# Kernel tuning notes

Hardware: AMD Instinct MI355X
Metric: run time of the kernel (lower is better)

The kernel has to match this reference:

```python
import jax, jax.numpy as jnp
import numpy as np

E = 500000          # num edges
V_IN = 128          # node feature dim
E_IN = 64           # edge feature dim
U_IN = 64           # global feature dim
HID = 256           # hidden_dim
NG = 512            # num graphs
CAT = 2 * V_IN + E_IN + U_IN  # 448


def setup_inputs() -> dict:
    key = jax.random.key(0)
    ks = jax.random.split(key, 8)
    return {
        "src": jax.random.normal(ks[0], (E, V_IN), dtype=jnp.float32),
        "dest": jax.random.normal(ks[1], (E, V_IN), dtype=jnp.float32),
        "edge_attr": jax.random.normal(ks[2], (E, E_IN), dtype=jnp.float32),
        "u": jax.random.normal(ks[3], (NG, U_IN), dtype=jnp.float32),
        "batch": jax.random.randint(ks[4], (E,), 0, NG, dtype=jnp.int64),
        "W1": jax.random.normal(ks[5], (CAT, HID), dtype=jnp.float32) * (1.0 / np.sqrt(CAT)),
        "b1": jnp.zeros((HID,), dtype=jnp.float32),
        "W2": jax.random.normal(ks[6], (HID, HID), dtype=jnp.float32) * (1.0 / np.sqrt(HID)),
        "b2": jnp.zeros((HID,), dtype=jnp.float32),
    }


def reference(src, dest, edge_attr, u, batch, W1, b1, W2, b2):
    # gather per-edge global features, concat, then 2-layer MLP with ReLU
    x = jnp.concatenate([src, dest, edge_attr, u[batch]], axis=1)  # [E, CAT]
    h = jax.nn.relu(x @ W1 + b1)                                   # [E, HID]
    return h @ W2 + b2                                             # [E, HID]
```

## Files before the change

kernel.cpp:

```cpp
#include <hip/hip_runtime.h>
#include <hip/hip_bf16.h>

#define E_EDGES 500000
#define V_IN 128
#define E_IN 64
#define U_IN 64
#define NG 512
#define HID 256
#define CAT 384
#define BM 64
#define BK 32
#define NCHUNK1 12
#define NCHUNK2 8
#define TILE 8192

typedef short short8 __attribute__((ext_vector_type(8)));
typedef float f32x4 __attribute__((ext_vector_type(4)));

static __device__ __forceinline__ short f2bf(float f) {
  unsigned u = __builtin_bit_cast(unsigned, f);
  u += 0x7fffu + ((u >> 16) & 1u);
  return (short)(u >> 16);
}

static __device__ __forceinline__ void gload_lds16(const void* g, void* l) {
  __builtin_amdgcn_global_load_lds(
      (const __attribute__((address_space(1))) unsigned int*)g,
      (unsigned int __attribute__((address_space(3)))*)l, 16, 0, 0);
}

static __device__ __forceinline__ void stage_w(const short* gsrc, short* lbase,
                                               int w, int l) {
#pragma unroll
  for (int i = 0; i < 4; ++i) {
    int off = (w * 4 + i) * 1024;
    gload_lds16((const char*)gsrc + off + l * 16, (char*)lbase + off);
  }
}

__global__ void prep_weights(const float* __restrict__ W1,
                             const float* __restrict__ W2,
                             short* __restrict__ w1t, short* __restrict__ w2t) {
  int idx = blockIdx.x * 256 + threadIdx.x;
  if (idx < CAT * HID) {
    int kc = idx >> 13;
    int rem = idx & (TILE - 1);
    int n = rem >> 5, kk = rem & 31;
    int swz = ((((kk >> 3) ^ (n & 3)) << 3) | (kk & 7));
    w1t[kc * TILE + n * 32 + swz] = f2bf(W1[(size_t)(kc * 32 + kk) * HID + n]);
  } else if (idx < CAT * HID + HID * HID) {
    int j = idx - CAT * HID;
    int kc = j >> 13;
    int rem = j & (TILE - 1);
    int n = rem >> 5, kk = rem & 31;
    int swz = ((((kk >> 3) ^ (n & 3)) << 3) | (kk & 7));
    w2t[kc * TILE + n * 32 + swz] = f2bf(W2[(size_t)(kc * 32 + kk) * HID + n]);
  }
}

__global__ __launch_bounds__(256, 2) void edge_mlp(
    const float* __restrict__ src, const float* __restrict__ dst,
    const float* __restrict__ edg, const float* __restrict__ u,
    const int* __restrict__ batch,
    const float* __restrict__ b1, const float* __restrict__ b2,
    const short* __restrict__ w1t, const short* __restrict__ w2t,
    float* __restrict__ out) {
  __shared__ short xs[BM][40];
  __shared__ short wsl[2][TILE];
  __shared__ short hs[BM][264];
  __shared__ float biasLds[2 * HID];

  const int t = threadIdx.x;
  const int l = t & 63;
  const int wc = t >> 6;
  const int l15 = l & 15, lg = l >> 4;
  const int r0 = blockIdx.x * BM;

  stage_w(w1t, wsl[0], wc, l);

  const int srow = t >> 2;
  const int cq = (t & 3) << 3;
  int gr = r0 + srow;
  if (gr >= E_EDGES) gr = E_EDGES - 1;
  int bi = batch[gr];
  bi = bi < 0 ? 0 : (bi >= NG ? NG - 1 : bi);
  const float* uptr = u + (size_t)bi * U_IN;
  const float* csrc[NCHUNK1] = {
      src + (size_t)gr * V_IN + cq,        src + (size_t)gr * V_IN + 32 + cq,
      src + (size_t)gr * V_IN + 64 + cq,   src + (size_t)gr * V_IN + 96 + cq,
      dst + (size_t)gr * V_IN + cq,        dst + (size_t)gr * V_IN + 32 + cq,
      dst + (size_t)gr * V_IN + 64 + cq,   dst + (size_t)gr * V_IN + 96 + cq,
      edg + (size_t)gr * E_IN + cq,        edg + (size_t)gr * E_IN + 32 + cq,
      uptr + cq,                           uptr + 32 + cq};

  f32x4 xv0, xv1;
  {
    const f32x4* p = (const f32x4*)csrc[0];
    xv0 = p[0]; xv1 = p[1];
  }

  biasLds[t] = b1[t];
  biasLds[t + HID] = b2[t];

  f32x4 acc[4][4];
#pragma unroll
  for (int m = 0; m < 4; ++m)
#pragma unroll
    for (int n = 0; n < 4; ++n)
#pragma unroll
      for (int j = 0; j < 4; ++j) acc[m][n][j] = 0.f;

#pragma unroll
  for (int kc = 0; kc < NCHUNK1; ++kc) {
    {
      short8 v;
      v[0] = f2bf(xv0[0]); v[1] = f2bf(xv0[1]); v[2] = f2bf(xv0[2]); v[3] = f2bf(xv0[3]);
      v[4] = f2bf(xv1[0]); v[5] = f2bf(xv1[1]); v[6] = f2bf(xv1[2]); v[7] = f2bf(xv1[3]);
      *(short8*)&xs[srow][cq] = v;
    }
    __syncthreads();

    f32x4 nx0, nx1;
    if (kc < NCHUNK1 - 1) {
      stage_w(w1t + (kc + 1) * TILE, wsl[(kc + 1) & 1], wc, l);
      const f32x4* p = (const f32x4*)csrc[kc + 1];
      nx0 = p[0]; nx1 = p[1];
    } else {
      stage_w(w2t, wsl[0], wc, l);
    }

    const short* wcur = wsl[kc & 1];
    short8 a[4], b[4];
#pragma unroll
    for (int m = 0; m < 4; ++m)
      a[m] = *(const short8*)&xs[m * 16 + l15][lg * 8];
#pragma unroll
    for (int n = 0; n < 4; ++n) {
      int nn = wc * 64 + n * 16 + l15;
      int blk = lg ^ (nn & 3);
      b[n] = *(const short8*)&wcur[nn * 32 + blk * 8];
    }
#pragma unroll
    for (int m = 0; m < 4; ++m)
#pragma unroll
      for (int n = 0; n < 4; ++n)
        acc[m][n] = __builtin_amdgcn_mfma_f32_16x16x32_bf16(a[m], b[n], acc[m][n], 0, 0, 0);

    __syncthreads();
    if (kc < NCHUNK1 - 1) { xv0 = nx0; xv1 = nx1; }
  }

#pragma unroll
  for (int n = 0; n < 4; ++n) {
    int col = wc * 64 + n * 16 + l15;
    float bv = biasLds[col];
#pragma unroll
    for (int m = 0; m < 4; ++m)
#pragma unroll
      for (int j = 0; j < 4; ++j) {
        int row = m * 16 + lg * 4 + j;
        float hv = acc[m][n][j] + bv;
        hs[row][col] = f2bf(fmaxf(hv, 0.f));
      }
  }

#pragma unroll
  for (int m = 0; m < 4; ++m)
#pragma unroll
    for (int n = 0; n < 4; ++n)
#pragma unroll
      for (int j = 0; j < 4; ++j) acc[m][n][j] = 0.f;

  __syncthreads();

#pragma unroll
  for (int kc = 0; kc < NCHUNK2; ++kc) {
    if (kc < NCHUNK2 - 1)
      stage_w(w2t + (kc + 1) * TILE, wsl[(kc + 1) & 1], wc, l);

    const short* wcur = wsl[kc & 1];
    short8 a[4], b[4];
#pragma unroll
    for (int m = 0; m < 4; ++m)
      a[m] = *(const short8*)&hs[m * 16 + l15][kc * 32 + lg * 8];
#pragma unroll
    for (int n = 0; n < 4; ++n) {
      int nn = wc * 64 + n * 16 + l15;
      int blk = lg ^ (nn & 3);
      b[n] = *(const short8*)&wcur[nn * 32 + blk * 8];
    }
#pragma unroll
    for (int m = 0; m < 4; ++m)
#pragma unroll
      for (int n = 0; n < 4; ++n)
        acc[m][n] = __builtin_amdgcn_mfma_f32_16x16x32_bf16(a[m], b[n], acc[m][n], 0, 0, 0);

    if (kc < NCHUNK2 - 1) __syncthreads();
  }

#pragma unroll
  for (int n = 0; n < 4; ++n) {
    int col = wc * 64 + n * 16 + l15;
    float bv = biasLds[HID + col];
#pragma unroll
    for (int m = 0; m < 4; ++m) {
      int rbase = r0 + m * 16 + lg * 4;
#pragma unroll
      for (int j = 0; j < 4; ++j) {
        int r = rbase + j;
        if (r < E_EDGES) out[(size_t)r * HID + col] = acc[m][n][j] + bv;
      }
    }
  }
}

extern "C" void kernel_launch(void* const* d_in, const int* in_sizes, int n_in,
                              void* d_out, int out_size, void* d_ws, size_t ws_size,
                              hipStream_t stream) {
  const float* src = (const float*)d_in[0];
  const float* dst = (const float*)d_in[1];
  const float* edg = (const float*)d_in[2];
  const float* u   = (const float*)d_in[3];
  const int* batch = (const int*)d_in[4];
  const float* W1 = (const float*)d_in[5];
  const float* b1 = (const float*)d_in[6];
  const float* W2 = (const float*)d_in[7];
  const float* b2 = (const float*)d_in[8];
  float* out = (float*)d_out;

  short* w1t = (short*)d_ws;
  short* w2t = w1t + CAT * HID;

  int prep_grid = (CAT * HID + HID * HID) / 256;
  prep_weights<<<prep_grid, 256, 0, stream>>>(W1, W2, w1t, w2t);

  int grid = (E_EDGES + BM - 1) / BM;
  edge_mlp<<<grid, 256, 0, stream>>>(src, dst, edg, u, batch, b1, b2, w1t, w2t, out);
}
```

Measured before the change: 1.097 ms.

## Load X fragments directly into registers with two-deep prefetch, drop LDS staging

Each lane now loads its own MFMA A-operand rows of the concatenated input straight from global memory into registers via inline asm, and converts them with packed bf16 conversion instructions. The xs LDS buffer and its write/sync round trip go away. X loads for chunk kc+2 are issued two chunks ahead, and hand-placed vmcnt/lgkmcnt waits with scheduling barriers control when loads and weight staging complete. In exchange the kernel holds more live registers and depends on manual waitcnt counts being correct, which may hurt occupancy or correctness.

```diff
diff --git a/kernel.cpp b/kernel.cpp
--- a/kernel.cpp
+++ b/kernel.cpp
@@ -9,13 +9,28 @@
 #define HID 256
 #define CAT 384
 #define BM 64
-#define BK 32
 #define NCHUNK1 12
 #define NCHUNK2 8
 #define TILE 8192
 
 typedef short short8 __attribute__((ext_vector_type(8)));
 typedef float f32x4 __attribute__((ext_vector_type(4)));
+
+#define WAITV(N)                                                    \
+  do {                                                              \
+    asm volatile("s_waitcnt vmcnt(" #N ")" ::: "memory");           \
+    __builtin_amdgcn_sched_barrier(0);                              \
+  } while (0)
+#define WAITLGKM0                                                   \
+  do {                                                              \
+    asm volatile("s_waitcnt lgkmcnt(0)" ::: "memory");              \
+    __builtin_amdgcn_sched_barrier(0);                              \
+  } while (0)
+#define BARR                                                        \
+  do {                                                              \
+    __builtin_amdgcn_s_barrier();                                   \
+    __builtin_amdgcn_sched_barrier(0);                              \
+  } while (0)
 
 static __device__ __forceinline__ short f2bf(float f) {
   unsigned u = __builtin_bit_cast(unsigned, f);
@@ -36,6 +51,24 @@
     int off = (w * 4 + i) * 1024;
     gload_lds16((const char*)gsrc + off + l * 16, (char*)lbase + off);
   }
+}
+
+static __device__ __forceinline__ void gl_x2(uint64_t addr, f32x4& d0, f32x4& d1) {
+  asm volatile(
+      "global_load_dwordx4 %0, %2, off\n\t"
+      "global_load_dwordx4 %1, %2, off offset:16"
+      : "=&v"(d0), "=&v"(d1)
+      : "v"(addr)
+      : "memory");
+}
+
+static __device__ __forceinline__ short8 cvt8(f32x4 a, f32x4 b) {
+  union { unsigned u[4]; short8 s; } r;
+  asm("v_cvt_pk_bf16_f32 %0, %1, %2" : "=v"(r.u[0]) : "v"(a[0]), "v"(a[1]));
+  asm("v_cvt_pk_bf16_f32 %0, %1, %2" : "=v"(r.u[1]) : "v"(a[2]), "v"(a[3]));
+  asm("v_cvt_pk_bf16_f32 %0, %1, %2" : "=v"(r.u[2]) : "v"(b[0]), "v"(b[1]));
+  asm("v_cvt_pk_bf16_f32 %0, %1, %2" : "=v"(r.u[3]) : "v"(b[2]), "v"(b[3]));
+  return r.s;
 }
 
 __global__ void prep_weights(const float* __restrict__ W1,
@@ -65,7 +98,6 @@
     const float* __restrict__ b1, const float* __restrict__ b2,
     const short* __restrict__ w1t, const short* __restrict__ w2t,
     float* __restrict__ out) {
-  __shared__ short xs[BM][40];
   __shared__ short wsl[2][TILE];
   __shared__ short hs[BM][264];
   __shared__ float biasLds[2 * HID];
@@ -76,32 +108,45 @@
   const int l15 = l & 15, lg = l >> 4;
   const int r0 = blockIdx.x * BM;
 
-  stage_w(w1t, wsl[0], wc, l);
-
-  const int srow = t >> 2;
-  const int cq = (t & 3) << 3;
-  int gr = r0 + srow;
-  if (gr >= E_EDGES) gr = E_EDGES - 1;
-  int bi = batch[gr];
-  bi = bi < 0 ? 0 : (bi >= NG ? NG - 1 : bi);
-  const float* uptr = u + (size_t)bi * U_IN;
-  const float* csrc[NCHUNK1] = {
-      src + (size_t)gr * V_IN + cq,        src + (size_t)gr * V_IN + 32 + cq,
-      src + (size_t)gr * V_IN + 64 + cq,   src + (size_t)gr * V_IN + 96 + cq,
-      dst + (size_t)gr * V_IN + cq,        dst + (size_t)gr * V_IN + 32 + cq,
-      dst + (size_t)gr * V_IN + 64 + cq,   dst + (size_t)gr * V_IN + 96 + cq,
-      edg + (size_t)gr * E_IN + cq,        edg + (size_t)gr * E_IN + 32 + cq,
-      uptr + cq,                           uptr + 32 + cq};
-
-  f32x4 xv0, xv1;
-  {
-    const f32x4* p = (const f32x4*)csrc[0];
-    xv0 = p[0]; xv1 = p[1];
-  }
-
   biasLds[t] = b1[t];
   biasLds[t + HID] = b2[t];
 
+  uint64_t rowkSD[4], rowkE[4], rowkU[4];
+#pragma unroll
+  for (int m = 0; m < 4; ++m) {
+    int gr = r0 + m * 16 + l15;
+    if (gr >= E_EDGES) gr = E_EDGES - 1;
+    int bi = batch[gr];
+    bi = bi < 0 ? 0 : (bi >= NG ? NG - 1 : bi);
+    rowkSD[m] = (uint64_t)gr * 512u + (unsigned)(lg * 32);
+    rowkE[m]  = (uint64_t)gr * 256u + (unsigned)(lg * 32);
+    rowkU[m]  = (uint64_t)(const char*)u + (uint64_t)bi * 256u + (unsigned)(lg * 32);
+  }
+  const uint64_t sbase = (uint64_t)(const char*)src;
+  const uint64_t dbase = (uint64_t)(const char*)dst;
+  const uint64_t ebase = (uint64_t)(const char*)edg;
+
+  WAITLGKM0;
+  BARR;
+
+  f32x4 xb[2][4][2];
+
+#define XADDR(kc_, m_)                                                       \
+  ((kc_) < 4    ? sbase + rowkSD[m_] + (uint64_t)((kc_)*128)                 \
+   : (kc_) < 8  ? dbase + rowkSD[m_] + (uint64_t)(((kc_)-4) * 128)           \
+   : (kc_) < 10 ? ebase + rowkE[m_] + (uint64_t)(((kc_)-8) * 128)            \
+                : rowkU[m_] + (uint64_t)(((kc_)-10) * 128))
+
+#define ISSUE_X(kc_)                                                         \
+  do {                                                                       \
+    _Pragma("unroll") for (int m = 0; m < 4; ++m)                            \
+        gl_x2(XADDR(kc_, m), xb[(kc_)&1][m][0], xb[(kc_)&1][m][1]);          \
+  } while (0)
+
+  stage_w(w1t, wsl[0], wc, l);
+  ISSUE_X(0);
+  ISSUE_X(1);
+
   f32x4 acc[4][4];
 #pragma unroll
   for (int m = 0; m < 4; ++m)
@@ -112,28 +157,21 @@
 
 #pragma unroll
   for (int kc = 0; kc < NCHUNK1; ++kc) {
-    {
-      short8 v;
-      v[0] = f2bf(xv0[0]); v[1] = f2bf(xv0[1]); v[2] = f2bf(xv0[2]); v[3] = f2bf(xv0[3]);
-      v[4] = f2bf(xv1[0]); v[5] = f2bf(xv1[1]); v[6] = f2bf(xv1[2]); v[7] = f2bf(xv1[3]);
-      *(short8*)&xs[srow][cq] = v;
-    }
-    __syncthreads();
-
-    f32x4 nx0, nx1;
-    if (kc < NCHUNK1 - 1) {
+    if (kc < NCHUNK1 - 1) WAITV(8); else WAITV(0);
+    short8 a[4];
+#pragma unroll
+    for (int m = 0; m < 4; ++m)
+      a[m] = cvt8(xb[kc & 1][m][0], xb[kc & 1][m][1]);
+    BARR;
+
+    if (kc < NCHUNK1 - 1)
       stage_w(w1t + (kc + 1) * TILE, wsl[(kc + 1) & 1], wc, l);
-      const f32x4* p = (const f32x4*)csrc[kc + 1];
-      nx0 = p[0]; nx1 = p[1];
-    } else {
+    else
       stage_w(w2t, wsl[0], wc, l);
-    }
+    if (kc < NCHUNK1 - 2) ISSUE_X(kc + 2);
 
     const short* wcur = wsl[kc & 1];
-    short8 a[4], b[4];
-#pragma unroll
-    for (int m = 0; m < 4; ++m)
-      a[m] = *(const short8*)&xs[m * 16 + l15][lg * 8];
+    short8 b[4];
 #pragma unroll
     for (int n = 0; n < 4; ++n) {
       int nn = wc * 64 + n * 16 + l15;
@@ -145,9 +183,7 @@
 #pragma unroll
       for (int n = 0; n < 4; ++n)
         acc[m][n] = __builtin_amdgcn_mfma_f32_16x16x32_bf16(a[m], b[n], acc[m][n], 0, 0, 0);
-
-    __syncthreads();
-    if (kc < NCHUNK1 - 1) { xv0 = nx0; xv1 = nx1; }
+    BARR;
   }
 
 #pragma unroll
@@ -159,11 +195,9 @@
 #pragma unroll
       for (int j = 0; j < 4; ++j) {
         int row = m * 16 + lg * 4 + j;
-        float hv = acc[m][n][j] + bv;
-        hs[row][col] = f2bf(fmaxf(hv, 0.f));
+        hs[row][col] = f2bf(fmaxf(acc[m][n][j] + bv, 0.f));
       }
   }
-
 #pragma unroll
   for (int m = 0; m < 4; ++m)
 #pragma unroll
@@ -171,10 +205,13 @@
 #pragma unroll
       for (int j = 0; j < 4; ++j) acc[m][n][j] = 0.f;
 
-  __syncthreads();
+  WAITLGKM0;
+  BARR;
 
 #pragma unroll
   for (int kc = 0; kc < NCHUNK2; ++kc) {
+    WAITV(0);
+    BARR;
     if (kc < NCHUNK2 - 1)
       stage_w(w2t + (kc + 1) * TILE, wsl[(kc + 1) & 1], wc, l);
 
@@ -194,8 +231,7 @@
 #pragma unroll
       for (int n = 0; n < 4; ++n)
         acc[m][n] = __builtin_amdgcn_mfma_f32_16x16x32_bf16(a[m], b[n], acc[m][n], 0, 0, 0);
-
-    if (kc < NCHUNK2 - 1) __syncthreads();
+    BARR;
   }
 
 #pragma unroll
```

Measured after the change: 1.223 ms. 11.5% more time.
